# Kernel optimization log

Measured on AMD Instinct MI355X. Metric: run time of the kernel, lower is better.

Reference implementation:

```python
import jax, jax.numpy as jnp
import numpy as np

K = 3  # kernel_size


def _unfold_patches(x, k):
    # torch x.unfold(2,k,1).unfold(3,k,1): shape (B, C, oh, ow, k, k)
    B, C, H, W = x.shape
    oh, ow = H - k + 1, W - k + 1
    rows = []
    for di in range(k):
        cols = [x[:, :, di:di + oh, dj:dj + ow] for dj in range(k)]
        rows.append(jnp.stack(cols, axis=-1))  # (B,C,oh,ow,k)
    return jnp.stack(rows, axis=-2)  # (B,C,oh,ow,k,k)


def setup_inputs() -> dict:
    key = jax.random.key(0)
    k1, k2 = jax.random.split(key)
    B, C_in, H, W = 16, 32, 224, 224
    C_out = 64
    in_features = C_in * K * K
    x = jax.random.normal(k1, (B, C_in, H, W), dtype=jnp.float32)
    weights = jax.random.normal(k2, (in_features, C_out), dtype=jnp.float32) / np.float32(in_features ** 0.5)
    bias = jnp.zeros((C_out,), dtype=jnp.float32)
    return {"x": x, "weights": weights, "bias": bias}


def reference(x, weights, bias):
    B, C, H, W = x.shape
    oh, ow = H - K + 1, W - K + 1
    patches = _unfold_patches(x, K)                  # (B,C,oh,ow,k,k)
    # Faithful to source: raw reshape of contiguous (B,C,oh,ow,k,k) buffer
    # to (B,oh,ow,C*k*k) -- NOT a channel permutation.
    patches = patches.reshape(B, oh, ow, -1)         # (B,oh,ow,C*k*k)
    out = patches @ weights + bias                   # (B,oh,ow,C_out)
    return jnp.transpose(out, (0, 3, 1, 2))          # (B,C_out,oh,ow)
```

## Files before the change

### kernel.cpp

```cpp
#include <hip/hip_runtime.h>
#include <hip/hip_bf16.h>
#include <stdint.h>

typedef __bf16 bf16_t;
typedef __bf16 bf16x8 __attribute__((ext_vector_type(8)));
typedef float  f32x4  __attribute__((ext_vector_type(4)));

constexpr int kOH = 222, kOW = 222;
constexpr int kS   = kOH * kOW;
constexpr int kCin = 32, kH = 224, kW = 224;
constexpr int kCout = 64;
constexpr int kK   = 288;
constexpr int kB   = 16;
constexpr int kM   = kB * kS;
constexpr int kBM  = 64;
constexpr int kLDK = 296;

__global__ void prep_weights(const float* __restrict__ w, bf16_t* __restrict__ wt) {
    int e = blockIdx.x * 256 + threadIdx.x;
    if (e >= kCout * kLDK) return;
    int n = e / kLDK, f = e - n * kLDK;
    float v = (f < kK) ? w[f * kCout + n] : 0.0f;
    wt[e] = (bf16_t)v;
}

__global__ __launch_bounds__(256) void conv_mfma(
        const float* __restrict__ x, const bf16_t* __restrict__ wt,
        const float* __restrict__ bias, float* __restrict__ out) {
    __shared__ __align__(16) bf16_t sA[kBM * kLDK];

    const int tid = threadIdx.x;
    const int m0  = blockIdx.x * kBM;

    #pragma unroll
    for (int it = 0; it < 8; ++it) {
        int pl = it * 256 + tid;
        int r  = pl >> 5;
        int t  = pl & 31;
        int m  = m0 + r;
        int b  = m / kS;
        int s  = m - b * kS;
        int pix = s * 32 + t;
        int c  = pix / kS;
        int pp = pix - c * kS;
        int ii = pp / kOW;
        int jj = pp - ii * kOW;
        const float* xp = x + ((b * kCin + c) * kH + ii) * kW + jj;
        bf16_t* ap = sA + r * kLDK + t * 9;
        #pragma unroll
        for (int di = 0; di < 3; ++di)
            #pragma unroll
            for (int dj = 0; dj < 3; ++dj)
                ap[di * 3 + dj] = (bf16_t)xp[di * kW + dj];
    }

    const int wv   = tid >> 6;
    const int lane = tid & 63;
    const int lc   = lane & 15;
    const int q    = lane >> 4;

    bf16x8 afr[9];
    #pragma unroll
    for (int ks = 0; ks < 9; ++ks) {
        const bf16_t* p = wt + (wv * 16 + lc) * kLDK + ks * 32 + q * 8;
        afr[ks] = *(const bf16x8*)p;
    }

    __syncthreads();

    f32x4 acc[4] = {};
    #pragma unroll
    for (int pg = 0; pg < 4; ++pg) {
        const bf16_t* bx = sA + (pg * 16 + lc) * kLDK;
        #pragma unroll
        for (int ks = 0; ks < 9; ++ks) {
            bf16x8 bfrag = *(const bf16x8*)(bx + ks * 32 + q * 8);
            acc[pg] = __builtin_amdgcn_mfma_f32_16x16x32_bf16(afr[ks], bfrag, acc[pg], 0, 0, 0);
        }
    }

    #pragma unroll
    for (int pg = 0; pg < 4; ++pg) {
        int m = m0 + pg * 16 + lc;
        int b = m / kS;
        int s = m - b * kS;
        float* op = out + (b * kCout) * kS + s;
        #pragma unroll
        for (int reg = 0; reg < 4; ++reg) {
            int n = wv * 16 + q * 4 + reg;
            op[n * kS] = acc[pg][reg] + bias[n];
        }
    }
}

extern "C" void kernel_launch(void* const* d_in, const int* in_sizes, int n_in,
                              void* d_out, int out_size, void* d_ws, size_t ws_size,
                              hipStream_t stream) {
    (void)in_sizes; (void)n_in; (void)out_size; (void)ws_size;
    const float* x    = (const float*)d_in[0];
    const float* w    = (const float*)d_in[1];
    const float* bias = (const float*)d_in[2];
    float*       out  = (float*)d_out;
    bf16_t*      wt   = (bf16_t*)d_ws;

    prep_weights<<<(kCout * kLDK + 255) / 256, 256, 0, stream>>>(w, wt);
    conv_mfma<<<kM / kBM, 256, 0, stream>>>(x, wt, bias, out);
}
```

Baseline: 379.4 us.

## Permute K to tap-major order and gather patches with vector loads

The weight prep now reorders the reduction dimension so that each tap holds 32 contiguous pixel positions. This lets the im2col gather read 8 consecutive floats with two float4 loads per task and write one 16-byte bf16 vector to shared memory, replacing 9 scalar loads and stores per position. Row wraparound is handled with a second load and a select, and addresses are clamped to stay in bounds. The padded LDS stride is dropped, which shrinks LDS but may raise bank conflicts, and launch bounds now request 4 blocks per CU.

After: 396.4 us. 4.5% more time.

```diff
diff --git a/kernel.cpp b/kernel.cpp
--- a/kernel.cpp
+++ b/kernel.cpp
@@ -5,53 +5,69 @@
 typedef __bf16 bf16_t;
 typedef __bf16 bf16x8 __attribute__((ext_vector_type(8)));
 typedef float  f32x4  __attribute__((ext_vector_type(4)));
+typedef float  f32x4u __attribute__((ext_vector_type(4), aligned(4)));
 
-constexpr int kOH = 222, kOW = 222;
-constexpr int kS   = kOH * kOW;
-constexpr int kCin = 32, kH = 224, kW = 224;
+constexpr int kS   = 49284;
 constexpr int kCout = 64;
 constexpr int kK   = 288;
 constexpr int kB   = 16;
 constexpr int kM   = kB * kS;
 constexpr int kBM  = 64;
-constexpr int kLDK = 296;
+constexpr int kImg = 32 * 224 * 224;
+constexpr unsigned kLim = (unsigned)kB * kImg - 8;
 
-__global__ void prep_weights(const float* __restrict__ w, bf16_t* __restrict__ wt) {
+__global__ void prep_weights(const float* __restrict__ w, bf16_t* __restrict__ wt2) {
     int e = blockIdx.x * 256 + threadIdx.x;
-    if (e >= kCout * kLDK) return;
-    int n = e / kLDK, f = e - n * kLDK;
-    float v = (f < kK) ? w[f * kCout + n] : 0.0f;
-    wt[e] = (bf16_t)v;
+    if (e >= kCout * kK) return;
+    int n = e / kK, kp = e - n * kK;
+    int tap = kp >> 5, t = kp & 31;
+    int f = t * 9 + tap;
+    wt2[e] = (bf16_t)w[f * kCout + n];
 }
 
-__global__ __launch_bounds__(256) void conv_mfma(
-        const float* __restrict__ x, const bf16_t* __restrict__ wt,
+__global__ __launch_bounds__(256, 4) void conv_mfma(
+        const float* __restrict__ x, const bf16_t* __restrict__ wt2,
         const float* __restrict__ bias, float* __restrict__ out) {
-    __shared__ __align__(16) bf16_t sA[kBM * kLDK];
+    __shared__ __align__(16) bf16_t sA[kBM * kK];
 
     const int tid = threadIdx.x;
     const int m0  = blockIdx.x * kBM;
 
     #pragma unroll
-    for (int it = 0; it < 8; ++it) {
-        int pl = it * 256 + tid;
-        int r  = pl >> 5;
-        int t  = pl & 31;
-        int m  = m0 + r;
-        int b  = m / kS;
-        int s  = m - b * kS;
-        int pix = s * 32 + t;
-        int c  = pix / kS;
-        int pp = pix - c * kS;
-        int ii = pp / kOW;
-        int jj = pp - ii * kOW;
-        const float* xp = x + ((b * kCin + c) * kH + ii) * kW + jj;
-        bf16_t* ap = sA + r * kLDK + t * 9;
+    for (int it = 0; it < 9; ++it) {
+        unsigned tsk = it * 256 + tid;
+        unsigned r   = tsk / 36u;
+        unsigned c36 = tsk - r * 36u;
+        unsigned tap = c36 >> 2, q8 = c36 & 3;
+        unsigned m   = m0 + r;
+        unsigned b   = m / (unsigned)kS;
+        unsigned s   = m - b * kS;
+        unsigned pix0 = s * 32u + q8 * 8u;
+        unsigned cc  = pix0 / (unsigned)kS;
+        unsigned rem = pix0 - cc * kS;
+        unsigned ii  = rem / 222u;
+        unsigned jj  = rem - ii * 222u;
+        unsigned A0  = pix0 + 892u * cc + 2u * ii;
+        int usplit   = 222 - (int)jj;
+        unsigned extra = (ii == 221u) ? 450u : 2u;
+        unsigned di  = tap / 3u, dj = tap - di * 3u;
+        unsigned fltA = b * (unsigned)kImg + A0 + di * 224u + dj;
+        fltA = min(fltA, kLim);
+        f32x4u a0 = *(const f32x4u*)(x + fltA);
+        f32x4u a1 = *(const f32x4u*)(x + fltA + 4);
+        f32x4u b0 = a0, b1 = a1;
+        if (usplit < 8) {
+            unsigned fltB = min(fltA + extra, kLim);
+            b0 = *(const f32x4u*)(x + fltB);
+            b1 = *(const f32x4u*)(x + fltB + 4);
+        }
+        float va[8] = {a0.x, a0.y, a0.z, a0.w, a1.x, a1.y, a1.z, a1.w};
+        float vb[8] = {b0.x, b0.y, b0.z, b0.w, b1.x, b1.y, b1.z, b1.w};
+        bf16x8 frag;
         #pragma unroll
-        for (int di = 0; di < 3; ++di)
-            #pragma unroll
-            for (int dj = 0; dj < 3; ++dj)
-                ap[di * 3 + dj] = (bf16_t)xp[di * kW + dj];
+        for (int u = 0; u < 8; ++u)
+            frag[u] = (bf16_t)((u < usplit) ? va[u] : vb[u]);
+        *(bf16x8*)(sA + r * kK + tap * 32u + q8 * 8u) = frag;
     }
 
     const int wv   = tid >> 6;
@@ -61,21 +77,19 @@
 
     bf16x8 afr[9];
     #pragma unroll
-    for (int ks = 0; ks < 9; ++ks) {
-        const bf16_t* p = wt + (wv * 16 + lc) * kLDK + ks * 32 + q * 8;
-        afr[ks] = *(const bf16x8*)p;
-    }
+    for (int tap = 0; tap < 9; ++tap)
+        afr[tap] = *(const bf16x8*)(wt2 + (wv * 16 + lc) * kK + tap * 32 + q * 8);
 
     __syncthreads();
 
     f32x4 acc[4] = {};
     #pragma unroll
     for (int pg = 0; pg < 4; ++pg) {
-        const bf16_t* bx = sA + (pg * 16 + lc) * kLDK;
+        const bf16_t* bx = sA + (pg * 16 + lc) * kK;
         #pragma unroll
-        for (int ks = 0; ks < 9; ++ks) {
-            bf16x8 bfrag = *(const bf16x8*)(bx + ks * 32 + q * 8);
-            acc[pg] = __builtin_amdgcn_mfma_f32_16x16x32_bf16(afr[ks], bfrag, acc[pg], 0, 0, 0);
+        for (int tap = 0; tap < 9; ++tap) {
+            bf16x8 bfrag = *(const bf16x8*)(bx + tap * 32 + q * 8);
+            acc[pg] = __builtin_amdgcn_mfma_f32_16x16x32_bf16(afr[tap], bfrag, acc[pg], 0, 0, 0);
         }
     }
 
@@ -101,8 +115,8 @@
     const float* w    = (const float*)d_in[1];
     const float* bias = (const float*)d_in[2];
     float*       out  = (float*)d_out;
-    bf16_t*      wt   = (bf16_t*)d_ws;
+    bf16_t*      wt2  = (bf16_t*)d_ws;
 
-    prep_weights<<<(kCout * kLDK + 255) / 256, 256, 0, stream>>>(w, wt);
-    conv_mfma<<<kM / kBM, 256, 0, stream>>>(x, wt, bias, out);
+    prep_weights<<<(kCout * kK + 255) / 256, 256, 0, stream>>>(w, wt2);
+    conv_mfma<<<kM / kBM, 256, 0, stream>>>(x, wt2, bias, out);
 }
```
